# Kernel optimization log

Measured on AMD Instinct MI355X. Metric: run time of the kernel, lower is better.

The kernel has to match this reference:

```python
import jax, jax.numpy as jnp
import numpy as np

N, M, ND, K = 80000, 150000, 10000, 27  # active voxels, 2D painted points, downscaled voxels, 3x3x3 kernel
C3, C2, CP = 16, 64, 259                # 3D ch (stage 1), 2D conv ch, painted 2D feature ch
CM, CO = C3 + C2, 32 + 64               # mixed ch (80), downscale out ch (96)


def subm_conv(feats, nbr, W):
    """Submanifold sparse conv as gather + per-offset GEMM.
    feats: [N_in, Cin], nbr: [N_out, K] int (-1 = missing), W: [K, Cin, Cout]."""
    out = jnp.zeros((nbr.shape[0], W.shape[-1]), feats.dtype)
    for k in range(W.shape[0]):  # fixed small kernel loop (27)
        idx = nbr[:, k]
        g = jnp.where((idx >= 0)[:, None], feats[jnp.clip(idx, 0)], 0.0)
        out = out + g @ W[k]
    return out


def bn_relu(x, gamma, beta):  # folded eval-mode BN1d + ReLU
    return jax.nn.relu(x * gamma + beta)


def setup_inputs() -> dict:
    key = jax.random.key(0)
    ks = jax.random.split(key, 24)

    def w(k, shape, fan_in):
        return jax.random.normal(k, shape, jnp.float32) * (1.0 / np.sqrt(fan_in))

    inp = {
        'x3d': jax.random.normal(ks[0], (N, C3), jnp.float32),
        'f2d': jax.random.normal(ks[1], (M, CP), jnp.float32),
        'nn_idx': jax.random.randint(ks[2], (N,), -1, M, jnp.int32),     # -1 = no 2D match
        'nbr': jax.random.randint(ks[3], (N, K), -1, N, jnp.int32),      # -1 = missing neighbor
        'nbr_ds': jax.random.randint(ks[4], (ND, K), -1, N, jnp.int32),
        'W3d': w(ks[5], (K, C3, C3), K * C3),
        'g3d': jnp.ones((C3,), jnp.float32), 'b3d': jnp.zeros((C3,), jnp.float32),
        'Wg': w(ks[6], (C3, CP), C3), 'bg': jnp.zeros((CP,), jnp.float32),
        'Wc': w(ks[7], (C3, CP), C3), 'bc': jnp.zeros((CP,), jnp.float32),
        'Wp': w(ks[8], (CP, C2), CP),
        'W2d': w(ks[9], (K, C2, C2), K * C2),
        'g2d': jnp.ones((C2,), jnp.float32), 'b2d': jnp.zeros((C2,), jnp.float32),
        'Wm1': w(ks[10], (K, CM, CM), K * CM),
        'gm1': jnp.ones((CM,), jnp.float32), 'bm1': jnp.zeros((CM,), jnp.float32),
        'Wm2': w(ks[11], (K, CM, CM), K * CM),
        'gm2': jnp.ones((CM,), jnp.float32), 'bm2': jnp.zeros((CM,), jnp.float32),
        'Wa1': w(ks[12], (K, CM, CM), K * CM),
        'ga1': jnp.ones((CM,), jnp.float32), 'ba1': jnp.zeros((CM,), jnp.float32),
        'Wa2': w(ks[13], (K, CM, CM), K * CM),
        'ga2': jnp.ones((CM,), jnp.float32), 'ba2': jnp.zeros((CM,), jnp.float32),
        'Wds': w(ks[14], (K, CM, CO), K * CM),
        'gds': jnp.ones((CO,), jnp.float32), 'bds': jnp.zeros((CO,), jnp.float32),
    }
    return inp


def reference(x3d, f2d, nn_idx, nbr, nbr_ds,
              W3d, g3d, b3d, Wg, bg, Wc, bc, Wp,
              W2d, g2d, b2d,
              Wm1, gm1, bm1, Wm2, gm2, bm2,
              Wa1, ga1, ba1, Wa2, ga2, ba2,
              Wds, gds, bds):
    # irregular gather of painted 2D features to voxel sites (NN index, -1 invalid)
    f2g = jnp.where((nn_idx >= 0)[:, None], f2d[jnp.clip(nn_idx, 0)], 0.0)  # [N, 259]

    # 3D branch: SubMConv3d(C3->C3) + BN + ReLU
    y3d = bn_relu(subm_conv(x3d, nbr, W3d), g3d, b3d)                       # [N, 16]

    # per-stage gate / cross-gate (Linear + ReLU) on 3D features, applied to raw 2D feats
    gate = jax.nn.relu(y3d @ Wg + bg)                                       # [N, 259]
    cross = jax.nn.relu(y3d @ Wc + bc)                                      # [N, 259]

    # gated 2D branch: project gated painted feats to 64, SubMConv3d + BN + ReLU
    p2d = (gate * f2g) @ Wp                                                 # [N, 64]
    x2d = bn_relu(subm_conv(p2d, nbr, W2d), g2d, b2d)                       # [N, 64]
    cross2d = (cross * f2g) @ Wp                                            # [N, 64]

    # cross-modal mix + SparseBasicBlock (residual, two subm convs)
    mix = jnp.concatenate([y3d, x2d + cross2d], axis=-1)                    # [N, 80]
    h = bn_relu(subm_conv(mix, nbr, Wm1), gm1, bm1)
    h = jax.nn.relu(subm_conv(h, nbr, Wm2) * gm2 + bm2 + mix)

    # aggregation SparseBasicBlock
    a = bn_relu(subm_conv(h, nbr, Wa1), ga1, ba1)
    a = jax.nn.relu(subm_conv(a, nbr, Wa2) * ga2 + ba2 + h)

    # strided SparseConv3d downscale (gather from input sites at new out sites)
    out = bn_relu(subm_conv(a, nbr_ds, Wds), gds, bds)                      # [ND, 96]
    return out
```

## Files before the change

kernel.cpp:

```cpp
#include <hip/hip_runtime.h>

#define NPTS 80000
#define MPTS 150000
#define NDPTS 10000
#define KOFF 27
#define C3 16
#define CP 259
#define C2 64
#define CM 80
#define CO 96

typedef __attribute__((ext_vector_type(8))) short short8;
typedef __attribute__((ext_vector_type(4))) float f32x4;

__device__ inline short bf16r(float f) {
  union { float f; unsigned u; } x{f};
  unsigned r = (x.u + 0x7fffu + ((x.u >> 16) & 1u)) >> 16;
  return (short)r;
}

__global__ void wfrag_kernel(const float* __restrict__ W, short* __restrict__ WbfF,
                             int CIN, int COUT_, int KC) {
  const int NT = COUT_ / 16;
  int i = blockIdx.x * 256 + threadIdx.x;
  int total = KOFF * KC * NT * 512;
  if (i >= total) return;
  int j = i & 7, lane = (i >> 3) & 63;
  int rest = i >> 9;
  int t = rest % NT; rest /= NT;
  int q = rest % KC;
  int k = rest / KC;
  int ci = q * 32 + (lane >> 4) * 8 + j;
  int n = t * 16 + (lane & 15);
  float v = (ci < CIN) ? W[((size_t)k * CIN + ci) * COUT_ + n] : 0.f;
  WbfF[i] = bf16r(v);
}

__global__ void wpfrag_kernel(const float* __restrict__ Wp, short* __restrict__ WpF) {
  int i = blockIdx.x * 256 + threadIdx.x;
  if (i >= 9 * 4 * 64 * 8) return;
  int j = i & 7, lane = (i >> 3) & 63, t = (i >> 9) & 3, q = i >> 11;
  int k = q * 32 + (lane >> 4) * 8 + j;
  int n = t * 16 + (lane & 15);
  WpF[i] = (k < CP) ? bf16r(Wp[(size_t)k * C2 + n]) : (short)0;
}

__global__ __launch_bounds__(256) void conv3d_bnrelu_kernel(
    const float* __restrict__ x3d, const int* __restrict__ nbr,
    const float* __restrict__ W3d, const float* __restrict__ g3d,
    const float* __restrict__ b3d, float* __restrict__ y3d,
    float* __restrict__ mix, short* __restrict__ mixbf)
{
  __shared__ float wS[KOFF * C3 * C3];
  __shared__ float fS[16][C3];
  const int tid = threadIdx.x;
  const int base = blockIdx.x * 16;
  for (int e = tid; e < KOFF * C3 * C3; e += 256) wS[e] = W3d[e];
  const int r = tid >> 4, c = tid & 15;
  const int row = base + r;
  float acc = 0.f;
  for (int k = 0; k < KOFF; ++k) {
    int idx = nbr[row * KOFF + k];
    float fv = (idx >= 0) ? x3d[idx * C3 + c] : 0.f;
    __syncthreads();
    fS[r][c] = fv;
    __syncthreads();
    const float* wk = &wS[k * C3 * C3];
    #pragma unroll
    for (int ci = 0; ci < C3; ++ci)
      acc = fmaf(fS[r][ci], wk[ci * C3 + c], acc);
  }
  float v = fmaxf(fmaf(acc, g3d[c], b3d[c]), 0.f);
  y3d[row * C3 + c] = v;
  mix[row * CM + c] = v;
  mixbf[row * CM + c] = bf16r(v);
}

__global__ __launch_bounds__(256) void gate_cross_mfma_kernel(
    const float* __restrict__ y3d, const float* __restrict__ f2d,
    const int* __restrict__ nn_idx,
    const float* __restrict__ Wg, const float* __restrict__ bg,
    const float* __restrict__ Wc, const float* __restrict__ bc,
    const short* __restrict__ WpF,
    short* __restrict__ p2dbf, float* __restrict__ cross2d)
{
  constexpr int RS = 296;
  __shared__ short g1S[32 * RS];
  __shared__ short g2S[32 * RS];
  const int tid = threadIdx.x;
  const int lane = tid & 63;
  const int w = tid >> 6;
  const int lm = lane & 15;
  const int quad = lane >> 4;
  const int base = blockIdx.x * 32;

  for (int e = tid; e < 32 * 32; e += 256) {
    int r = e >> 5, cc = 256 + (e & 31);
    if (cc >= CP) {
      g1S[r * RS + cc] = 0;
      g2S[r * RS + cc] = 0;
    }
  }

  {
    const int c = tid;
    float wg[16], wc[16];
    #pragma unroll
    for (int ci = 0; ci < 16; ++ci) {
      wg[ci] = Wg[ci * CP + c];
      wc[ci] = Wc[ci * CP + c];
    }
    const float bgv = bg[c], bcv = bc[c];
    for (int r = 0; r < 32; ++r) {
      const int row = base + r;
      const int idx = nn_idx[row];
      const float* yr = y3d + (size_t)row * C3;
      float f = (idx >= 0) ? f2d[(size_t)idx * CP + c] : 0.f;
      float a1 = bgv, a2 = bcv;
      #pragma unroll
      for (int ci = 0; ci < 16; ++ci) {
        float yv = yr[ci];
        a1 = fmaf(yv, wg[ci], a1);
        a2 = fmaf(yv, wc[ci], a2);
      }
      g1S[r * RS + c] = bf16r(fmaxf(a1, 0.f) * f);
      g2S[r * RS + c] = bf16r(fmaxf(a2, 0.f) * f);
    }
  }
  if (w == 0 && lane < 3) {
    const int c = 256 + lane;
    float wg[16], wc[16];
    #pragma unroll
    for (int ci = 0; ci < 16; ++ci) {
      wg[ci] = Wg[ci * CP + c];
      wc[ci] = Wc[ci * CP + c];
    }
    const float bgv = bg[c], bcv = bc[c];
    for (int r = 0; r < 32; ++r) {
      const int row = base + r;
      const int idx = nn_idx[row];
      const float* yr = y3d + (size_t)row * C3;
      float f = (idx >= 0) ? f2d[(size_t)idx * CP + c] : 0.f;
      float a1 = bgv, a2 = bcv;
      #pragma unroll
      for (int ci = 0; ci < 16; ++ci) {
        float yv = yr[ci];
        a1 = fmaf(yv, wg[ci], a1);
        a2 = fmaf(yv, wc[ci], a2);
      }
      g1S[r * RS + c] = bf16r(fmaxf(a1, 0.f) * f);
      g2S[r * RS + c] = bf16r(fmaxf(a2, 0.f) * f);
    }
  }
  __syncthreads();

  const int gsel = w & 1;
  const int mt = w >> 1;
  const short* gS = gsel ? g2S : g1S;
  f32x4 acc[4];
  #pragma unroll
  for (int t = 0; t < 4; ++t) {
    f32x4 z = {0.f, 0.f, 0.f, 0.f};
    acc[t] = z;
  }
  #pragma unroll
  for (int q = 0; q < 9; ++q) {
    short8 af = *(const short8*)&gS[(mt * 16 + lm) * RS + q * 32 + quad * 8];
    #pragma unroll
    for (int t = 0; t < 4; ++t) {
      short8 bf = *(const short8*)&WpF[(((q * 4 + t) * 64) + lane) * 8];
      acc[t] = __builtin_amdgcn_mfma_f32_16x16x32_bf16(af, bf, acc[t], 0, 0, 0);
    }
  }
  #pragma unroll
  for (int t = 0; t < 4; ++t) {
    const int c = t * 16 + lm;
    #pragma unroll
    for (int rg = 0; rg < 4; ++rg) {
      const int row = base + mt * 16 + quad * 4 + rg;
      float v = acc[t][rg];
      if (gsel == 0)
        p2dbf[(size_t)row * C2 + c] = bf16r(v);
      else
        cross2d[(size_t)row * C2 + c] = v;
    }
  }
}

template <int CIN, int COUT_, int MODE>
__global__ __launch_bounds__(64, 2) void conv_nolds_kernel(
    const short* __restrict__ finbf, const int* __restrict__ nbr, int nrows,
    const short* __restrict__ WbfF, const float* __restrict__ gamma,
    const float* __restrict__ beta, const float* __restrict__ resf,
    float* __restrict__ outf, short* __restrict__ outbf)
{
  constexpr int KC = (CIN + 31) / 32;
  constexpr int DCH = CIN / 8;
  constexpr int NT = COUT_ / 16;
  constexpr int MT = 2;

  const int lane = threadIdx.x;
  const int lm = lane & 15;
  const int quad = lane >> 4;
  const int base = blockIdx.x * (MT * 16);

  int rrow[MT];
  bool rok[MT];
  #pragma unroll
  for (int i = 0; i < MT; ++i) {
    rrow[i] = base + i * 16 + lm;
    rok[i] = rrow[i] < nrows;
  }

  f32x4 acc[MT][NT];
  #pragma unroll
  for (int i = 0; i < MT; ++i)
    #pragma unroll
    for (int t = 0; t < NT; ++t) {
      f32x4 z = {0.f, 0.f, 0.f, 0.f};
      acc[i][t] = z;
    }

  const short8 zero8 = {0, 0, 0, 0, 0, 0, 0, 0};

  auto loadIdx = [&](int (&id)[MT], int k) {
    #pragma unroll
    for (int i = 0; i < MT; ++i)
      id[i] = (k < KOFF && rok[i]) ? nbr[(size_t)rrow[i] * KOFF + k] : -1;
  };

  auto loadA = [&](short8 (&pa)[MT][KC], const int (&id)[MT]) {
    #pragma unroll
    for (int i = 0; i < MT; ++i) {
      const int safe = (id[i] < 0) ? 0 : id[i];
      const bool ok = id[i] >= 0;
      const short* src = finbf + (size_t)safe * CIN;
      #pragma unroll
      for (int q = 0; q < KC; ++q) {
        const int ch = q * 4 + quad;
        short8 v = zero8;
        if (ch < DCH) v = *(const short8*)(src + ch * 8);
        pa[i][q] = ok ? v : zero8;
      }
    }
  };

  auto computeK = [&](const short8 (&pa)[MT][KC], int k) {
    const short* wb = WbfF + ((size_t)k * KC * NT) * 512 + lane * 8;
    #pragma unroll
    for (int q = 0; q < KC; ++q) {
      #pragma unroll
      for (int t = 0; t < NT; ++t) {
        short8 bfr = *(const short8*)(wb + (q * NT + t) * 512);
        #pragma unroll
        for (int i = 0; i < MT; ++i)
          acc[i][t] = __builtin_amdgcn_mfma_f32_16x16x32_bf16(pa[i][q], bfr,
                                                              acc[i][t], 0, 0, 0);
      }
    }
  };

  int ia[MT], ib[MT], ic[MT];
  short8 paA[MT][KC], paB[MT][KC], paC[MT][KC];

  loadIdx(ia, 0); loadIdx(ib, 1); loadIdx(ic, 2);
  loadA(paA, ia); loadIdx(ia, 3);
  loadA(paB, ib); loadIdx(ib, 4);

  for (int kk = 0; kk < KOFF; kk += 3) {
    loadA(paC, ic); loadIdx(ic, kk + 5);
    computeK(paA, kk);
    loadA(paA, ia); loadIdx(ia, kk + 6);
    computeK(paB, kk + 1);
    loadA(paB, ib); loadIdx(ib, kk + 7);
    computeK(paC, kk + 2);
  }

  #pragma unroll
  for (int i = 0; i < MT; ++i) {
    int rbase = base + i * 16 + quad * 4;
    #pragma unroll
    for (int t = 0; t < NT; ++t) {
      int c = t * 16 + lm;
      float g = gamma[c], b = beta[c];
      #pragma unroll
      for (int rg = 0; rg < 4; ++rg) {
        int row = rbase + rg;
        if (row >= nrows) continue;
        float v = acc[i][t][rg];
        if (MODE == 0) {
          outf[(size_t)row * COUT_ + c] = fmaxf(fmaf(v, g, b), 0.f);
        } else if (MODE == 1) {
          outbf[(size_t)row * COUT_ + c] = bf16r(fmaxf(fmaf(v, g, b), 0.f));
        } else if (MODE == 2) {
          float o = fmaxf(fmaf(v, g, b), 0.f) + resf[(size_t)row * C2 + c];
          outf[(size_t)row * CM + 16 + c] = o;
          outbf[(size_t)row * CM + 16 + c] = bf16r(o);
        } else if (MODE == 3) {
          float o = fmaxf(fmaf(v, g, b) + resf[(size_t)row * COUT_ + c], 0.f);
          outf[(size_t)row * COUT_ + c] = o;
          outbf[(size_t)row * COUT_ + c] = bf16r(o);
        } else {
          float o = fmaxf(fmaf(v, g, b) + resf[(size_t)row * COUT_ + c], 0.f);
          outbf[(size_t)row * COUT_ + c] = bf16r(o);
        }
      }
    }
  }
}

extern "C" void kernel_launch(void* const* d_in, const int* in_sizes, int n_in,
                              void* d_out, int out_size, void* d_ws, size_t ws_size,
                              hipStream_t stream) {
  const float* x3d  = (const float*)d_in[0];
  const float* f2d  = (const float*)d_in[1];
  const int*   nn   = (const int*)d_in[2];
  const int*   nbr  = (const int*)d_in[3];
  const int*   nbds = (const int*)d_in[4];
  const float* W3d  = (const float*)d_in[5];
  const float* g3d  = (const float*)d_in[6];
  const float* b3d  = (const float*)d_in[7];
  const float* Wg   = (const float*)d_in[8];
  const float* bg   = (const float*)d_in[9];
  const float* Wc   = (const float*)d_in[10];
  const float* bc   = (const float*)d_in[11];
  const float* Wp   = (const float*)d_in[12];
  const float* W2d  = (const float*)d_in[13];
  const float* g2d  = (const float*)d_in[14];
  const float* b2d  = (const float*)d_in[15];
  const float* Wm1  = (const float*)d_in[16];
  const float* gm1  = (const float*)d_in[17];
  const float* bm1  = (const float*)d_in[18];
  const float* Wm2  = (const float*)d_in[19];
  const float* gm2  = (const float*)d_in[20];
  const float* bm2  = (const float*)d_in[21];
  const float* Wa1  = (const float*)d_in[22];
  const float* ga1  = (const float*)d_in[23];
  const float* ba1  = (const float*)d_in[24];
  const float* Wa2  = (const float*)d_in[25];
  const float* ga2  = (const float*)d_in[26];
  const float* ba2  = (const float*)d_in[27];
  const float* Wds  = (const float*)d_in[28];
  const float* gds  = (const float*)d_in[29];
  const float* bds  = (const float*)d_in[30];

  const size_t N = NPTS;
  float* ws = (float*)d_ws;
  float* y3d     = ws;
  short* p2dbf   = (short*)(ws + N * 16);
  float* cross2d = ws + N * 48;
  float* mix     = ws + N * 112;
  short* mixbf   = (short*)(ws + N * 192);
  short* tmp1bf  = (short*)(ws + N * 232);
  float* hbuf    = ws + N * 272;
  short* hbufbf  = (short*)(ws + N * 352);
  short* abufbf  = (short*)ws;
  short* wtail  = (short*)(ws + N * 392);
  short* WbfF2d = wtail;
  short* WbfFm1 = WbfF2d + 110592;
  short* WbfFm2 = WbfFm1 + 207360;
  short* WbfFa1 = WbfFm2 + 207360;
  short* WbfFa2 = WbfFa1 + 207360;
  short* WbfFds = WbfFa2 + 207360;
  short* WpF    = WbfFds + 248832;

  wfrag_kernel<<<(110592 + 255) / 256, 256, 0, stream>>>(W2d, WbfF2d, 64, 64, 2);
  wfrag_kernel<<<(207360 + 255) / 256, 256, 0, stream>>>(Wm1, WbfFm1, 80, 80, 3);
  wfrag_kernel<<<(207360 + 255) / 256, 256, 0, stream>>>(Wm2, WbfFm2, 80, 80, 3);
  wfrag_kernel<<<(207360 + 255) / 256, 256, 0, stream>>>(Wa1, WbfFa1, 80, 80, 3);
  wfrag_kernel<<<(207360 + 255) / 256, 256, 0, stream>>>(Wa2, WbfFa2, 80, 80, 3);
  wfrag_kernel<<<(248832 + 255) / 256, 256, 0, stream>>>(Wds, WbfFds, 80, 96, 3);
  wpfrag_kernel<<<(9 * 4 * 64 * 8 + 255) / 256, 256, 0, stream>>>(Wp, WpF);

  conv3d_bnrelu_kernel<<<NPTS / 16, 256, 0, stream>>>(x3d, nbr, W3d, g3d, b3d,
                                                      y3d, mix, mixbf);
  gate_cross_mfma_kernel<<<NPTS / 32, 256, 0, stream>>>(y3d, f2d, nn, Wg, bg,
                                                        Wc, bc, WpF, p2dbf,
                                                        cross2d);

  const int gridW = (NPTS + 31) / 32;
  conv_nolds_kernel<64, 64, 2><<<gridW, 64, 0, stream>>>(
      p2dbf, nbr, NPTS, WbfF2d, g2d, b2d, cross2d, mix, mixbf);
  conv_nolds_kernel<80, 80, 1><<<gridW, 64, 0, stream>>>(
      mixbf, nbr, NPTS, WbfFm1, gm1, bm1, nullptr, nullptr, tmp1bf);
  conv_nolds_kernel<80, 80, 3><<<gridW, 64, 0, stream>>>(
      tmp1bf, nbr, NPTS, WbfFm2, gm2, bm2, mix, hbuf, hbufbf);
  conv_nolds_kernel<80, 80, 1><<<gridW, 64, 0, stream>>>(
      hbufbf, nbr, NPTS, WbfFa1, ga1, ba1, nullptr, nullptr, tmp1bf);
  conv_nolds_kernel<80, 80, 4><<<gridW, 64, 0, stream>>>(
      tmp1bf, nbr, NPTS, WbfFa2, ga2, ba2, hbuf, nullptr, abufbf);

  const int gridDS = (NDPTS + 31) / 32;
  conv_nolds_kernel<80, 96, 0><<<gridDS, 64, 0, stream>>>(
      abufbf, nbds, NDPTS, WbfFds, gds, bds, nullptr, (float*)d_out, nullptr);
}
```

Before: 1.094 ms.

## Deepen gather prefetch pipeline in sparse convs and restructure gate/stage-1 loads

The MFMA sparse-conv kernel now processes one 16-row tile per wave, keeps a 6-deep register ring of prefetched neighbor gathers, and uses scheduling barriers and a higher occupancy hint. The aim is to hide the latency of the random gathers. The 3D conv double-buffers its shared feature tile with prefetch two offsets ahead, which removes one barrier per offset. The gate kernel issues all f2d gathers up front, stages y3d in shared memory, and spreads the 3 tail channels across 96 threads. The cost is higher register pressure, with possible spills, and weight fragments are no longer reused across two row tiles.

After: 1.994 ms. +82.3%, slower.

```diff
diff --git a/kernel.cpp b/kernel.cpp
--- a/kernel.cpp
+++ b/kernel.cpp
@@ -52,23 +52,33 @@
     float* __restrict__ mix, short* __restrict__ mixbf)
 {
   __shared__ float wS[KOFF * C3 * C3];
-  __shared__ float fS[16][C3];
+  __shared__ float fS[2][16][C3];
   const int tid = threadIdx.x;
   const int base = blockIdx.x * 16;
   for (int e = tid; e < KOFF * C3 * C3; e += 256) wS[e] = W3d[e];
   const int r = tid >> 4, c = tid & 15;
   const int row = base + r;
+
+  int i0 = nbr[row * KOFF + 0];
+  float fv = (i0 >= 0) ? x3d[i0 * C3 + c] : 0.f;
+  int i1 = nbr[row * KOFF + 1];
+  float fvn = (i1 >= 0) ? x3d[i1 * C3 + c] : 0.f;
+
   float acc = 0.f;
   for (int k = 0; k < KOFF; ++k) {
-    int idx = nbr[row * KOFF + k];
-    float fv = (idx >= 0) ? x3d[idx * C3 + c] : 0.f;
-    __syncthreads();
-    fS[r][c] = fv;
+    fS[k & 1][r][c] = fv;
+    fv = fvn;
+    if (k + 2 < KOFF) {
+      int ix = nbr[row * KOFF + k + 2];
+      fvn = (ix >= 0) ? x3d[ix * C3 + c] : 0.f;
+    } else {
+      fvn = 0.f;
+    }
     __syncthreads();
     const float* wk = &wS[k * C3 * C3];
     #pragma unroll
     for (int ci = 0; ci < C3; ++ci)
-      acc = fmaf(fS[r][ci], wk[ci * C3 + c], acc);
+      acc = fmaf(fS[k & 1][r][ci], wk[ci * C3 + c], acc);
   }
   float v = fmaxf(fmaf(acc, g3d[c], b3d[c]), 0.f);
   y3d[row * C3 + c] = v;
@@ -87,6 +97,7 @@
   constexpr int RS = 296;
   __shared__ short g1S[32 * RS];
   __shared__ short g2S[32 * RS];
+  __shared__ float yS[32][C3];
   const int tid = threadIdx.x;
   const int lane = tid & 63;
   const int w = tid >> 6;
@@ -102,55 +113,60 @@
     }
   }
 
-  {
-    const int c = tid;
-    float wg[16], wc[16];
+  int ix[32];
+  #pragma unroll
+  for (int r = 0; r < 32; ++r) ix[r] = nn_idx[base + r];
+
+  const int c = tid;
+  float f[32];
+  #pragma unroll
+  for (int r = 0; r < 32; ++r)
+    f[r] = (ix[r] >= 0) ? f2d[(size_t)ix[r] * CP + c] : 0.f;
+
+  float ftail = 0.f;
+  int tr = 0, tcc = 0;
+  if (tid < 96) {
+    tr = tid / 3; tcc = tid - tr * 3;
+    if (ix[tr] >= 0) ftail = f2d[(size_t)ix[tr] * CP + 256 + tcc];
+  }
+
+  for (int e = tid; e < 32 * C3; e += 256)
+    ((float*)yS)[e] = y3d[(size_t)base * C3 + e];
+
+  float wg[16], wc[16];
+  #pragma unroll
+  for (int ci = 0; ci < 16; ++ci) {
+    wg[ci] = Wg[ci * CP + c];
+    wc[ci] = Wc[ci * CP + c];
+  }
+  const float bgv = bg[c], bcv = bc[c];
+
+  __syncthreads();
+
+  #pragma unroll
+  for (int r = 0; r < 32; ++r) {
+    float a1 = bgv, a2 = bcv;
     #pragma unroll
     for (int ci = 0; ci < 16; ++ci) {
-      wg[ci] = Wg[ci * CP + c];
-      wc[ci] = Wc[ci * CP + c];
-    }
-    const float bgv = bg[c], bcv = bc[c];
-    for (int r = 0; r < 32; ++r) {
-      const int row = base + r;
-      const int idx = nn_idx[row];
-      const float* yr = y3d + (size_t)row * C3;
-      float f = (idx >= 0) ? f2d[(size_t)idx * CP + c] : 0.f;
-      float a1 = bgv, a2 = bcv;
-      #pragma unroll
-      for (int ci = 0; ci < 16; ++ci) {
-        float yv = yr[ci];
-        a1 = fmaf(yv, wg[ci], a1);
-        a2 = fmaf(yv, wc[ci], a2);
-      }
-      g1S[r * RS + c] = bf16r(fmaxf(a1, 0.f) * f);
-      g2S[r * RS + c] = bf16r(fmaxf(a2, 0.f) * f);
-    }
-  }
-  if (w == 0 && lane < 3) {
-    const int c = 256 + lane;
-    float wg[16], wc[16];
+      float yv = yS[r][ci];
+      a1 = fmaf(yv, wg[ci], a1);
+      a2 = fmaf(yv, wc[ci], a2);
+    }
+    g1S[r * RS + c] = bf16r(fmaxf(a1, 0.f) * f[r]);
+    g2S[r * RS + c] = bf16r(fmaxf(a2, 0.f) * f[r]);
+  }
+
+  if (tid < 96) {
+    const int c2 = 256 + tcc;
+    float a1 = bg[c2], a2 = bc[c2];
     #pragma unroll
     for (int ci = 0; ci < 16; ++ci) {
-      wg[ci] = Wg[ci * CP + c];
-      wc[ci] = Wc[ci * CP + c];
-    }
-    const float bgv = bg[c], bcv = bc[c];
-    for (int r = 0; r < 32; ++r) {
-      const int row = base + r;
-      const int idx = nn_idx[row];
-      const float* yr = y3d + (size_t)row * C3;
-      float f = (idx >= 0) ? f2d[(size_t)idx * CP + c] : 0.f;
-      float a1 = bgv, a2 = bcv;
-      #pragma unroll
-      for (int ci = 0; ci < 16; ++ci) {
-        float yv = yr[ci];
-        a1 = fmaf(yv, wg[ci], a1);
-        a2 = fmaf(yv, wc[ci], a2);
-      }
-      g1S[r * RS + c] = bf16r(fmaxf(a1, 0.f) * f);
-      g2S[r * RS + c] = bf16r(fmaxf(a2, 0.f) * f);
-    }
+      float yv = yS[tr][ci];
+      a1 = fmaf(yv, Wg[ci * CP + c2], a1);
+      a2 = fmaf(yv, Wc[ci * CP + c2], a2);
+    }
+    g1S[tr * RS + c2] = bf16r(fmaxf(a1, 0.f) * ftail);
+    g2S[tr * RS + c2] = bf16r(fmaxf(a2, 0.f) * ftail);
   }
   __syncthreads();
 
@@ -174,21 +190,21 @@
   }
   #pragma unroll
   for (int t = 0; t < 4; ++t) {
-    const int c = t * 16 + lm;
+    const int cc = t * 16 + lm;
     #pragma unroll
     for (int rg = 0; rg < 4; ++rg) {
       const int row = base + mt * 16 + quad * 4 + rg;
       float v = acc[t][rg];
       if (gsel == 0)
-        p2dbf[(size_t)row * C2 + c] = bf16r(v);
+        p2dbf[(size_t)row * C2 + cc] = bf16r(v);
       else
-        cross2d[(size_t)row * C2 + c] = v;
+        cross2d[(size_t)row * C2 + cc] = v;
     }
   }
 }
 
 template <int CIN, int COUT_, int MODE>
-__global__ __launch_bounds__(64, 2) void conv_nolds_kernel(
+__global__ __launch_bounds__(64, 3) void conv_pipe_kernel(
     const short* __restrict__ finbf, const int* __restrict__ nbr, int nrows,
     const short* __restrict__ WbfF, const float* __restrict__ gamma,
     const float* __restrict__ beta, const float* __restrict__ resf,
@@ -197,112 +213,99 @@
   constexpr int KC = (CIN + 31) / 32;
   constexpr int DCH = CIN / 8;
   constexpr int NT = COUT_ / 16;
-  constexpr int MT = 2;
+  constexpr int D = 6;
 
   const int lane = threadIdx.x;
   const int lm = lane & 15;
   const int quad = lane >> 4;
-  const int base = blockIdx.x * (MT * 16);
-
-  int rrow[MT];
-  bool rok[MT];
-  #pragma unroll
-  for (int i = 0; i < MT; ++i) {
-    rrow[i] = base + i * 16 + lm;
-    rok[i] = rrow[i] < nrows;
-  }
-
-  f32x4 acc[MT][NT];
-  #pragma unroll
-  for (int i = 0; i < MT; ++i)
-    #pragma unroll
-    for (int t = 0; t < NT; ++t) {
-      f32x4 z = {0.f, 0.f, 0.f, 0.f};
-      acc[i][t] = z;
-    }
+  const int base = blockIdx.x * 16;
+  const int row = base + lm;
+  const bool rok = row < nrows;
+
+  f32x4 acc[NT];
+  #pragma unroll
+  for (int t = 0; t < NT; ++t) {
+    f32x4 z = {0.f, 0.f, 0.f, 0.f};
+    acc[t] = z;
+  }
 
   const short8 zero8 = {0, 0, 0, 0, 0, 0, 0, 0};
-
-  auto loadIdx = [&](int (&id)[MT], int k) {
-    #pragma unroll
-    for (int i = 0; i < MT; ++i)
-      id[i] = (k < KOFF && rok[i]) ? nbr[(size_t)rrow[i] * KOFF + k] : -1;
+  short8 pa[D][KC];
+  int id[D];
+
+  auto loadIdx = [&](int k) -> int {
+    return (rok && k < KOFF) ? nbr[(size_t)row * KOFF + k] : -1;
   };
-
-  auto loadA = [&](short8 (&pa)[MT][KC], const int (&id)[MT]) {
-    #pragma unroll
-    for (int i = 0; i < MT; ++i) {
-      const int safe = (id[i] < 0) ? 0 : id[i];
-      const bool ok = id[i] >= 0;
-      const short* src = finbf + (size_t)safe * CIN;
-      #pragma unroll
-      for (int q = 0; q < KC; ++q) {
-        const int ch = q * 4 + quad;
-        short8 v = zero8;
-        if (ch < DCH) v = *(const short8*)(src + ch * 8);
-        pa[i][q] = ok ? v : zero8;
-      }
+  auto loadA = [&](short8 (&p)[KC], int idx) {
+    const int safe = (idx < 0) ? 0 : idx;
+    const short* src = finbf + (size_t)safe * CIN;
+    #pragma unroll
+    for (int q = 0; q < KC; ++q) {
+      const int ch = q * 4 + quad;
+      short8 v = zero8;
+      if (idx >= 0 && ch < DCH) v = *(const short8*)(src + ch * 8);
+      p[q] = v;
     }
   };
-
-  auto computeK = [&](const short8 (&pa)[MT][KC], int k) {
-    const short* wb = WbfF + ((size_t)k * KC * NT) * 512 + lane * 8;
+  auto computeK = [&](const short8 (&p)[KC], int k) {
+    const short* wb = WbfF + (size_t)(k * KC * NT) * 512 + lane * 8;
     #pragma unroll
     for (int q = 0; q < KC; ++q) {
       #pragma unroll
       for (int t = 0; t < NT; ++t) {
         short8 bfr = *(const short8*)(wb + (q * NT + t) * 512);
-        #pragma unroll
-        for (int i = 0; i < MT; ++i)
-          acc[i][t] = __builtin_amdgcn_mfma_f32_16x16x32_bf16(pa[i][q], bfr,
-                                                              acc[i][t], 0, 0, 0);
+        acc[t] = __builtin_amdgcn_mfma_f32_16x16x32_bf16(p[q], bfr, acc[t], 0, 0, 0);
       }
     }
   };
 
-  int ia[MT], ib[MT], ic[MT];
-  short8 paA[MT][KC], paB[MT][KC], paC[MT][KC];
-
-  loadIdx(ia, 0); loadIdx(ib, 1); loadIdx(ic, 2);
-  loadA(paA, ia); loadIdx(ia, 3);
-  loadA(paB, ib); loadIdx(ib, 4);
-
-  for (int kk = 0; kk < KOFF; kk += 3) {
-    loadA(paC, ic); loadIdx(ic, kk + 5);
-    computeK(paA, kk);
-    loadA(paA, ia); loadIdx(ia, kk + 6);
-    computeK(paB, kk + 1);
-    loadA(paB, ib); loadIdx(ib, kk + 7);
-    computeK(paC, kk + 2);
-  }
-
-  #pragma unroll
-  for (int i = 0; i < MT; ++i) {
-    int rbase = base + i * 16 + quad * 4;
+  #pragma unroll
+  for (int j = 0; j < D; ++j) {
+    int ixt = loadIdx(j);
+    loadA(pa[j], ixt);
+    id[j] = loadIdx(j + D);
+  }
+  __builtin_amdgcn_sched_barrier(0);
+
+  for (int kk = 0; kk < 24; kk += 6) {
+    #pragma unroll
+    for (int j = 0; j < D; ++j) {
+      computeK(pa[j], kk + j);
+      __builtin_amdgcn_sched_barrier(0);
+      loadA(pa[j], id[j]);
+      id[j] = loadIdx(kk + j + 2 * D);
+      __builtin_amdgcn_sched_barrier(0);
+    }
+  }
+  #pragma unroll
+  for (int j = 0; j < 3; ++j) computeK(pa[j], 24 + j);
+
+  {
+    const int rbase = base + quad * 4;
     #pragma unroll
     for (int t = 0; t < NT; ++t) {
-      int c = t * 16 + lm;
-      float g = gamma[c], b = beta[c];
+      const int cc = t * 16 + lm;
+      float g = gamma[cc], b = beta[cc];
       #pragma unroll
       for (int rg = 0; rg < 4; ++rg) {
-        int row = rbase + rg;
-        if (row >= nrows) continue;
-        float v = acc[i][t][rg];
+        int orow = rbase + rg;
+        if (orow >= nrows) continue;
+        float v = acc[t][rg];
         if (MODE == 0) {
-          outf[(size_t)row * COUT_ + c] = fmaxf(fmaf(v, g, b), 0.f);
+          outf[(size_t)orow * COUT_ + cc] = fmaxf(fmaf(v, g, b), 0.f);
         } else if (MODE == 1) {
-          outbf[(size_t)row * COUT_ + c] = bf16r(fmaxf(fmaf(v, g, b), 0.f));
+          outbf[(size_t)orow * COUT_ + cc] = bf16r(fmaxf(fmaf(v, g, b), 0.f));
         } else if (MODE == 2) {
-          float o = fmaxf(fmaf(v, g, b), 0.f) + resf[(size_t)row * C2 + c];
-          outf[(size_t)row * CM + 16 + c] = o;
-          outbf[(size_t)row * CM + 16 + c] = bf16r(o);
+          float o = fmaxf(fmaf(v, g, b), 0.f) + resf[(size_t)orow * C2 + cc];
+          outf[(size_t)orow * CM + 16 + cc] = o;
+          outbf[(size_t)orow * CM + 16 + cc] = bf16r(o);
         } else if (MODE == 3) {
-          float o = fmaxf(fmaf(v, g, b) + resf[(size_t)row * COUT_ + c], 0.f);
-          outf[(size_t)row * COUT_ + c] = o;
-          outbf[(size_t)row * COUT_ + c] = bf16r(o);
+          float o = fmaxf(fmaf(v, g, b) + resf[(size_t)orow * COUT_ + cc], 0.f);
+          outf[(size_t)orow * COUT_ + cc] = o;
+          outbf[(size_t)orow * COUT_ + cc] = bf16r(o);
         } else {
-          float o = fmaxf(fmaf(v, g, b) + resf[(size_t)row * COUT_ + c], 0.f);
-          outbf[(size_t)row * COUT_ + c] = bf16r(o);
+          float o = fmaxf(fmaf(v, g, b) + resf[(size_t)orow * COUT_ + cc], 0.f);
+          outbf[(size_t)orow * COUT_ + cc] = bf16r(o);
         }
       }
     }
@@ -378,19 +381,19 @@
                                                         Wc, bc, WpF, p2dbf,
                                                         cross2d);
 
-  const int gridW = (NPTS + 31) / 32;
-  conv_nolds_kernel<64, 64, 2><<<gridW, 64, 0, stream>>>(
+  const int gridW = (NPTS + 15) / 16;
+  conv_pipe_kernel<64, 64, 2><<<gridW, 64, 0, stream>>>(
       p2dbf, nbr, NPTS, WbfF2d, g2d, b2d, cross2d, mix, mixbf);
-  conv_nolds_kernel<80, 80, 1><<<gridW, 64, 0, stream>>>(
+  conv_pipe_kernel<80, 80, 1><<<gridW, 64, 0, stream>>>(
       mixbf, nbr, NPTS, WbfFm1, gm1, bm1, nullptr, nullptr, tmp1bf);
-  conv_nolds_kernel<80, 80, 3><<<gridW, 64, 0, stream>>>(
+  conv_pipe_kernel<80, 80, 3><<<gridW, 64, 0, stream>>>(
       tmp1bf, nbr, NPTS, WbfFm2, gm2, bm2, mix, hbuf, hbufbf);
-  conv_nolds_kernel<80, 80, 1><<<gridW, 64, 0, stream>>>(
+  conv_pipe_kernel<80, 80, 1><<<gridW, 64, 0, stream>>>(
       hbufbf, nbr, NPTS, WbfFa1, ga1, ba1, nullptr, nullptr, tmp1bf);
-  conv_nolds_kernel<80, 80, 4><<<gridW, 64, 0, stream>>>(
+  conv_pipe_kernel<80, 80, 4><<<gridW, 64, 0, stream>>>(
       tmp1bf, nbr, NPTS, WbfFa2, ga2, ba2, hbuf, nullptr, abufbf);
 
-  const int gridDS = (NDPTS + 31) / 32;
-  conv_nolds_kernel<80, 96, 0><<<gridDS, 64, 0, stream>>>(
+  const int gridDS = (NDPTS + 15) / 16;
+  conv_pipe_kernel<80, 96, 0><<<gridDS, 64, 0, stream>>>(
       abufbf, nbds, NDPTS, WbfFds, gds, bds, nullptr, (float*)d_out, nullptr);
 }
```
